# Kernel tuning notes

Hardware: AMD Instinct MI355X
Metric: run time of the kernel (lower is better)

## Reference

```python
import jax, jax.numpy as jnp
import numpy as np

H = 8          # head_num
NEG = -1e9     # mask fill value
LN_EPS = 1e-6


def setup_inputs() -> dict:
    key = jax.random.key(0)
    ks = jax.random.split(key, 12)
    B, S, D = 8, 1024, 512
    inp = {
        'q': jax.random.normal(ks[0], (B, S, D), jnp.float32),
        'k': jax.random.normal(ks[1], (B, S, D), jnp.float32),
        'v': jax.random.normal(ks[2], (B, S, D), jnp.float32),
        'query_mask': jax.random.randint(ks[3], (B, S), 0, 2, jnp.int32),
        'key_mask': jax.random.randint(ks[4], (B, S), 0, 2, jnp.int32),
        'Wq': jax.random.normal(ks[5], (D, D), jnp.float32) / np.sqrt(D),
        'bq': jax.random.normal(ks[6], (D,), jnp.float32) * 0.02,
        'Wk': jax.random.normal(ks[7], (D, D), jnp.float32) / np.sqrt(D),
        'bk': jax.random.normal(ks[8], (D,), jnp.float32) * 0.02,
        'Wv': jax.random.normal(ks[9], (D, D), jnp.float32) / np.sqrt(D),
        'bv': jax.random.normal(ks[10], (D,), jnp.float32) * 0.02,
        'gamma': jnp.ones((D,), jnp.float32),
        'beta': jnp.zeros((D,), jnp.float32),
    }
    return inp


def _to_batches(x):
    # [B,S,D] -> [B*H, S, D/H]  (batch-major head layout, as in torch code)
    B, S, D = x.shape
    return x.reshape(B, S, H, D // H).transpose(0, 2, 1, 3).reshape(B * H, S, D // H)


def _from_batches(x):
    BH, S, d = x.shape
    B = BH // H
    return x.reshape(B, H, S, d).transpose(0, 2, 1, 3).reshape(B, S, H * d)


def reference(q, k, v, query_mask, key_mask, Wq, bq, Wk, bk, Wv, bv, gamma, beta):
    # QKV linears + ReLU activation (activation=F.relu in original)
    _q = jax.nn.relu(q @ Wq.T + bq)
    _k = jax.nn.relu(k @ Wk.T + bk)
    _v = jax.nn.relu(v @ Wv.T + bv)
    _q, _k, _v = _to_batches(_q), _to_batches(_k), _to_batches(_v)  # [B*H,S,d]

    # masks tiled head-MAJOR (repeat(head_num,1) semantics): index = h*B + b
    km = jnp.tile(key_mask, (H, 1))[:, None, :]    # [B*H, 1, S_k]
    qm = jnp.tile(query_mask, (H, 1))[:, :, None]  # [B*H, S_q, 1]

    d = _q.shape[-1]
    scores = jnp.einsum('bqd,bkd->bqk', _q, _k) / jnp.sqrt(jnp.float32(d))
    scores = jnp.where(km == 0, NEG, scores)
    attn = jax.nn.softmax(scores, axis=-1)
    attn = attn * qm.astype(attn.dtype)            # multiplicative query mask
    # dropout: eval mode (rate applied only in training) -> identity
    y = jnp.einsum('bqk,bkd->bqd', attn, _v)
    y = _from_batches(y) + q                       # residual
    # LayerNorm over last dim
    mu = jnp.mean(y, axis=-1, keepdims=True)
    var = jnp.mean((y - mu) ** 2, axis=-1, keepdims=True)
    return gamma * (y - mu) / jnp.sqrt(var + LN_EPS) + beta
```

## Files before the change

kernel.cpp:

```cpp
#include <hip/hip_runtime.h>
#include <hip/hip_bf16.h>
#include <stdint.h>

constexpr int kB = 8, kH = 8, kS = 1024, kD = 512, kDH = 64;
constexpr float kNeg = -1e9f;
constexpr float kScaleLog2e = 0.125f * 1.4426950408889634f;

typedef __attribute__((ext_vector_type(8))) short bf16x8;
typedef __attribute__((ext_vector_type(8))) unsigned short u16x8;
typedef __attribute__((ext_vector_type(4))) float f32x4;
typedef __attribute__((ext_vector_type(4))) unsigned short u16x4;

__device__ __forceinline__ unsigned short f2bf(float f) {
  union { float f; unsigned int u; } a; a.f = f;
  return (unsigned short)((a.u + 0x7FFFu + ((a.u >> 16) & 1u)) >> 16);
}
__device__ __forceinline__ float bf2f(unsigned short u) {
  union { unsigned int u; float f; } a; a.u = ((unsigned int)u) << 16;
  return a.f;
}
__device__ __forceinline__ unsigned int pk2bf(float lo, float hi) {
  union { __hip_bfloat162 h; unsigned int u; } cv;
  cv.h = __float22bfloat162_rn(make_float2(lo, hi));
  return cv.u;
}
__device__ __forceinline__ uint4 gload16(const void* p) {
  uint4 r;
  asm volatile("global_load_dwordx4 %0, %1, off" : "=v"(r) : "v"(p));
  return r;
}
__device__ __forceinline__ int gload4(const void* p) {
  int r;
  asm volatile("global_load_dword %0, %1, off" : "=v"(r) : "v"(p));
  return r;
}
#define WAIT_VMCNT(N) do { \
  asm volatile("s_waitcnt vmcnt(" #N ")" ::: "memory"); \
  __builtin_amdgcn_sched_barrier(0); } while (0)

__device__ __forceinline__ uint4 cvt4(uint4 a, uint4 b) {
  uint4 r;
  r.x = pk2bf(__uint_as_float(a.x), __uint_as_float(a.y));
  r.y = pk2bf(__uint_as_float(a.z), __uint_as_float(a.w));
  r.z = pk2bf(__uint_as_float(b.x), __uint_as_float(b.y));
  r.w = pk2bf(__uint_as_float(b.z), __uint_as_float(b.w));
  return r;
}

#if __has_builtin(__builtin_amdgcn_exp2f)
#define EXP2F(x) __builtin_amdgcn_exp2f(x)
#else
#define EXP2F(x) exp2f(x)
#endif

__global__ __launch_bounds__(256)
void wcvt_kernel(const float* __restrict__ wq, const float* __restrict__ wk,
                 const float* __restrict__ wv, unsigned short* __restrict__ wout)
{
  const int tid = blockIdx.x * 256 + threadIdx.x;
  const int z = tid >> 16;
  const int i = (tid & 65535) * 4;
  const float* W = (z == 0) ? wq : (z == 1) ? wk : wv;
  float4 v4 = *(const float4*)(W + i);
  u16x4 pk;
  pk[0] = f2bf(v4.x); pk[1] = f2bf(v4.y); pk[2] = f2bf(v4.z); pk[3] = f2bf(v4.w);
  *(u16x4*)(wout + (size_t)z * 262144 + i) = pk;
}

__global__ __launch_bounds__(256)
void qkv_gemm_kernel(const float* __restrict__ xq, const float* __restrict__ xk,
                     const float* __restrict__ xv,
                     const unsigned short* __restrict__ wbf,
                     const float* __restrict__ bq, const float* __restrict__ bk,
                     const float* __restrict__ bv,
                     unsigned short* __restrict__ wsout)
{
  __shared__ __align__(16) unsigned short As[2][128][72];
  __shared__ __align__(16) unsigned short Bs[2][128][72];

  const int bid = blockIdx.x;
  const int xcd = bid & 7;
  const int j = bid >> 3;
  const int x = j & 3;
  const int g = (j >> 2) * 8 + xcd;
  const int z = g >> 6;
  const int y = g & 63;

  const float* X    = (z == 0) ? xq : (z == 1) ? xk : xv;
  const unsigned short* Wb = wbf + (size_t)z * 262144;
  const float* bias = (z == 0) ? bq : (z == 1) ? bk : bv;
  unsigned short* out = wsout + (size_t)z * (kB * kS * kD);

  const int m0 = y * 128;
  const int n0 = x * 128;
  const int t = threadIdx.x;
  const int lane = t & 63;
  const int w = t >> 6;
  const int wr = w >> 1, wc = w & 1;
  const int l16 = lane & 15, lg = lane >> 4;

  const int row = t >> 3, c8 = (t & 7) * 8;
  const float* Xr = X + (size_t)(m0 + row) * kD + c8;
  const unsigned short* Wr = Wb + (size_t)(n0 + row) * kD + c8;

  f32x4 acc[4][4] = {};
  uint4 pa0, pa1, pa2, pa3, pa4, pa5, pa6, pa7, pb0, pb1, pb2, pb3;
  uint4 qa0, qa1, qa2, qa3, qa4, qa5, qa6, qa7, qb0, qb1, qb2, qb3;

  auto issueP = [&](int kt) {
    pa0 = gload16(Xr + kt);            pa1 = gload16(Xr + kt + 4);
    pa2 = gload16(Xr + 32 * kD + kt);  pa3 = gload16(Xr + 32 * kD + kt + 4);
    pa4 = gload16(Xr + 64 * kD + kt);  pa5 = gload16(Xr + 64 * kD + kt + 4);
    pa6 = gload16(Xr + 96 * kD + kt);  pa7 = gload16(Xr + 96 * kD + kt + 4);
    pb0 = gload16(Wr + kt);            pb1 = gload16(Wr + 32 * kD + kt);
    pb2 = gload16(Wr + 64 * kD + kt);  pb3 = gload16(Wr + 96 * kD + kt);
  };
  auto issueQ = [&](int kt) {
    qa0 = gload16(Xr + kt);            qa1 = gload16(Xr + kt + 4);
    qa2 = gload16(Xr + 32 * kD + kt);  qa3 = gload16(Xr + 32 * kD + kt + 4);
    qa4 = gload16(Xr + 64 * kD + kt);  qa5 = gload16(Xr + 64 * kD + kt + 4);
    qa6 = gload16(Xr + 96 * kD + kt);  qa7 = gload16(Xr + 96 * kD + kt + 4);
    qb0 = gload16(Wr + kt);            qb1 = gload16(Wr + 32 * kD + kt);
    qb2 = gload16(Wr + 64 * kD + kt);  qb3 = gload16(Wr + 96 * kD + kt);
  };
  auto writeP = [&]() {
    *(uint4*)&As[0][row][c8]      = cvt4(pa0, pa1);
    *(uint4*)&As[0][row + 32][c8] = cvt4(pa2, pa3);
    *(uint4*)&As[0][row + 64][c8] = cvt4(pa4, pa5);
    *(uint4*)&As[0][row + 96][c8] = cvt4(pa6, pa7);
    *(uint4*)&Bs[0][row][c8]      = pb0;
    *(uint4*)&Bs[0][row + 32][c8] = pb1;
    *(uint4*)&Bs[0][row + 64][c8] = pb2;
    *(uint4*)&Bs[0][row + 96][c8] = pb3;
  };
  auto writeQ = [&]() {
    *(uint4*)&As[1][row][c8]      = cvt4(qa0, qa1);
    *(uint4*)&As[1][row + 32][c8] = cvt4(qa2, qa3);
    *(uint4*)&As[1][row + 64][c8] = cvt4(qa4, qa5);
    *(uint4*)&As[1][row + 96][c8] = cvt4(qa6, qa7);
    *(uint4*)&Bs[1][row][c8]      = qb0;
    *(uint4*)&Bs[1][row + 32][c8] = qb1;
    *(uint4*)&Bs[1][row + 64][c8] = qb2;
    *(uint4*)&Bs[1][row + 96][c8] = qb3;
  };
  auto mfma_phase = [&](int buf) {
#pragma unroll
    for (int kk = 0; kk < 2; ++kk) {
      bf16x8 av[4], bv[4];
#pragma unroll
      for (int mf = 0; mf < 4; ++mf)
        av[mf] = *(const bf16x8*)&As[buf][wr * 64 + mf * 16 + l16][kk * 32 + lg * 8];
#pragma unroll
      for (int nf = 0; nf < 4; ++nf)
        bv[nf] = *(const bf16x8*)&Bs[buf][wc * 64 + nf * 16 + l16][kk * 32 + lg * 8];
#pragma unroll
      for (int nf = 0; nf < 4; ++nf)
#pragma unroll
        for (int mf = 0; mf < 4; ++mf)
          acc[mf][nf] = __builtin_amdgcn_mfma_f32_16x16x32_bf16(bv[nf], av[mf], acc[mf][nf], 0, 0, 0);
    }
  };

  issueP(0);
  issueQ(64);
#pragma unroll
  for (int i = 0; i < 6; i += 2) {
    WAIT_VMCNT(12);
    writeP();
    issueP((i + 2) * 64);
    __syncthreads();
    mfma_phase(0);
    WAIT_VMCNT(12);
    writeQ();
    issueQ((i + 3) * 64);
    __syncthreads();
    mfma_phase(1);
  }
  WAIT_VMCNT(12);
  writeP();
  __syncthreads();
  mfma_phase(0);
  WAIT_VMCNT(0);
  writeQ();
  __syncthreads();
  mfma_phase(1);

  if (z == 2) {
    const int mmbase = m0 + wr * 64;
    const int b_ = mmbase >> 10, sbase = mmbase & 1023;
#pragma unroll
    for (int nf = 0; nf < 4; ++nf) {
#pragma unroll
      for (int r = 0; r < 4; ++r) {
        const int n = n0 + wc * 64 + nf * 16 + lg * 4 + r;
        const float bval = bias[n];
        const int h = n >> 6, dd = n & 63;
        u16x4 pk;
#pragma unroll
        for (int mf = 0; mf < 4; ++mf) {
          float vv = acc[mf][nf][r] + bval;
          vv = vv > 0.f ? vv : 0.f;
          pk[mf] = f2bf(vv);
        }
        *(u16x4*)&out[((size_t)((b_ * kH + h) * kDH + dd)) * kS + sbase + l16 * 4] = pk;
      }
    }
  } else {
#pragma unroll
    for (int mf = 0; mf < 4; ++mf) {
      const int mm = m0 + wr * 64 + mf * 16 + l16;
      const int b_ = mm >> 10, s = mm & 1023;
#pragma unroll
      for (int nf = 0; nf < 4; ++nf) {
        const int nbase = n0 + wc * 64 + nf * 16 + lg * 4;
        const int h = nbase >> 6, dd = nbase & 63;
        u16x4 pk;
#pragma unroll
        for (int r = 0; r < 4; ++r) {
          float vv = acc[mf][nf][r] + bias[nbase + r];
          vv = vv > 0.f ? vv : 0.f;
          pk[r] = f2bf(vv);
        }
        *(u16x4*)&out[((size_t)(b_ * kH + h) * kS + s) * kDH + dd] = pk;
      }
    }
  }
}

__global__ __launch_bounds__(256)
void attn_kernel(const unsigned short* __restrict__ ws,
                 const int* __restrict__ key_mask,
                 unsigned short* __restrict__ ybf)
{
  __shared__ __align__(16) unsigned short Ks[2][64][72];
  __shared__ __align__(16) unsigned short Vts[2][64][72];
  __shared__ __align__(16) unsigned short Ps[4][32][72];
  __shared__ float kmadd[2][64];

  const unsigned short* Qw = ws;
  const unsigned short* Kw = ws + (size_t)1 * kB * kS * kD;
  const unsigned short* Vw = ws + (size_t)2 * kB * kS * kD;

  const int bid = blockIdx.x;
  const int xcd = bid & 7;
  const int j = bid >> 3;
  const int qx = j & 7;
  const int bh = (j >> 3) * 8 + xcd;

  const int q0 = qx * 128;
  const int t = threadIdx.x;
  const int w = t >> 6, lane = t & 63;
  const int l16 = lane & 15, lg = lane >> 4;
  const int b_ = bh / kH, h = bh % kH;

  const unsigned short* Qb = Qw + ((size_t)bh * kS + q0) * kDH;
  const unsigned short* Kb = Kw + (size_t)bh * kS * kDH;
  const unsigned short* Vb = Vw + (size_t)bh * kDH * kS;
  const int* km = key_mask + (bh % kB) * kS;

  const int srow = t >> 3, sc8 = (t & 7) * 8;
  const unsigned short* KbR0 = Kb + (size_t)srow * kDH + sc8;
  const unsigned short* KbR1 = Kb + (size_t)(srow + 32) * kDH + sc8;
  const unsigned short* VbR0 = Vb + (size_t)srow * kS + sc8;
  const unsigned short* VbR1 = Vb + (size_t)(srow + 32) * kS + sc8;

  bf16x8 aq[2][2];
#pragma unroll
  for (int u = 0; u < 2; ++u)
#pragma unroll
    for (int kk = 0; kk < 2; ++kk)
      aq[u][kk] = *(const bf16x8*)(Qb + (size_t)(w * 32 + u * 16 + l16) * kDH + kk * 32 + lg * 8);

  bf16x8 vone;
#pragma unroll
  for (int jj = 0; jj < 8; ++jj) vone[jj] = (short)0x3F80;

  f32x4 o[2][4] = {};
  f32x4 lacc[2] = {};

  uint4 ka0, ka1, va0, va1; int kma;
  uint4 kb0, kb1, vb0, vb1; int kmb;

  auto issueA = [&](int kv0) {
    ka0 = gload16(KbR0 + (size_t)kv0 * kDH);
    ka1 = gload16(KbR1 + (size_t)kv0 * kDH);
    va0 = gload16(VbR0 + kv0);
    va1 = gload16(VbR1 + kv0);
    kma = gload4(km + kv0 + (t & 63));
  };
  auto issueB = [&](int kv0) {
    kb0 = gload16(KbR0 + (size_t)kv0 * kDH);
    kb1 = gload16(KbR1 + (size_t)kv0 * kDH);
    vb0 = gload16(VbR0 + kv0);
    vb1 = gload16(VbR1 + kv0);
    kmb = gload4(km + kv0 + (t & 63));
  };
  auto writeA = [&]() {
    *(uint4*)&Ks[0][srow][sc8]       = ka0;
    *(uint4*)&Ks[0][srow + 32][sc8]  = ka1;
    *(uint4*)&Vts[0][srow][sc8]      = va0;
    *(uint4*)&Vts[0][srow + 32][sc8] = va1;
    if (t < 64) kmadd[0][t] = kma ? 0.f : kNeg;
  };
  auto writeB = [&]() {
    *(uint4*)&Ks[1][srow][sc8]       = kb0;
    *(uint4*)&Ks[1][srow + 32][sc8]  = kb1;
    *(uint4*)&Vts[1][srow][sc8]      = vb0;
    *(uint4*)&Vts[1][srow + 32][sc8] = vb1;
    if (t < 64) kmadd[1][t] = kmb ? 0.f : kNeg;
  };
  auto compute = [&](int buf) {
    f32x4 sc[2][4] = {};
    __builtin_amdgcn_s_setprio(1);
#pragma unroll
    for (int kk = 0; kk < 2; ++kk) {
#pragma unroll
      for (int nf = 0; nf < 4; ++nf) {
        bf16x8 bfr = *(const bf16x8*)&Ks[buf][nf * 16 + l16][kk * 32 + lg * 8];
#pragma unroll
        for (int u = 0; u < 2; ++u)
          sc[u][nf] = __builtin_amdgcn_mfma_f32_16x16x32_bf16(aq[u][kk], bfr, sc[u][nf], 0, 0, 0);
      }
    }
    __builtin_amdgcn_s_setprio(0);
    float madd[4];
#pragma unroll
    for (int nf = 0; nf < 4; ++nf) madd[nf] = kmadd[buf][nf * 16 + l16];
#pragma unroll
    for (int u = 0; u < 2; ++u) {
#pragma unroll
      for (int r = 0; r < 4; ++r) {
        const float p0 = EXP2F(fmaf(sc[u][0][r], kScaleLog2e, madd[0]));
        const float p1 = EXP2F(fmaf(sc[u][1][r], kScaleLog2e, madd[1]));
        const float p2 = EXP2F(fmaf(sc[u][2][r], kScaleLog2e, madd[2]));
        const float p3 = EXP2F(fmaf(sc[u][3][r], kScaleLog2e, madd[3]));
        const int prow = u * 16 + lg * 4 + r;
        uint2 pw;
        pw.x = __builtin_amdgcn_perm(__float_as_uint(p1), __float_as_uint(p0), 0x07060302u);
        pw.y = __builtin_amdgcn_perm(__float_as_uint(p3), __float_as_uint(p2), 0x07060302u);
        *(uint2*)&Ps[w][prow][l16 * 4] = pw;
      }
    }
    __builtin_amdgcn_s_setprio(1);
#pragma unroll
    for (int kk = 0; kk < 2; ++kk) {
      bf16x8 a0 = *(const bf16x8*)&Ps[w][l16][kk * 32 + lg * 8];
      bf16x8 a1 = *(const bf16x8*)&Ps[w][16 + l16][kk * 32 + lg * 8];
#pragma unroll
      for (int nd = 0; nd < 4; ++nd) {
        bf16x8 bfr = *(const bf16x8*)&Vts[buf][nd * 16 + l16][kk * 32 + lg * 8];
        o[0][nd] = __builtin_amdgcn_mfma_f32_16x16x32_bf16(a0, bfr, o[0][nd], 0, 0, 0);
        o[1][nd] = __builtin_amdgcn_mfma_f32_16x16x32_bf16(a1, bfr, o[1][nd], 0, 0, 0);
      }
      lacc[0] = __builtin_amdgcn_mfma_f32_16x16x32_bf16(a0, vone, lacc[0], 0, 0, 0);
      lacc[1] = __builtin_amdgcn_mfma_f32_16x16x32_bf16(a1, vone, lacc[1], 0, 0, 0);
    }
    __builtin_amdgcn_s_setprio(0);
  };

  issueA(0);
  issueB(64);
  for (int i = 0; i < 14; i += 2) {
    WAIT_VMCNT(5);
    writeA();
    issueA((i + 2) * 64);
    __syncthreads();
    compute(0);
    WAIT_VMCNT(5);
    writeB();
    issueB((i + 3) * 64);
    __syncthreads();
    compute(1);
  }
  WAIT_VMCNT(5);
  writeA();
  __syncthreads();
  compute(0);
  WAIT_VMCNT(0);
  writeB();
  __syncthreads();
  compute(1);

#pragma unroll
  for (int u = 0; u < 2; ++u) {
    float rinv[4];
#pragma unroll
    for (int r = 0; r < 4; ++r) rinv[r] = 1.f / lacc[u][r];
#pragma unroll
    for (int nd = 0; nd < 4; ++nd) {
#pragma unroll
      for (int r = 0; r < 4; ++r) {
        const int srowq = q0 + w * 32 + u * 16 + lg * 4 + r;
        ybf[((size_t)b_ * kS + srowq) * kD + h * kDH + nd * 16 + l16] =
            f2bf(o[u][nd][r] * rinv[r]);
      }
    }
  }
}

__global__ __launch_bounds__(256)
void ln_kernel(const unsigned short* __restrict__ ybf, const float* __restrict__ q,
               const int* __restrict__ qmask,
               const float* __restrict__ gamma, const float* __restrict__ beta,
               float* __restrict__ out)
{
  const int w = threadIdx.x >> 6, lane = threadIdx.x & 63;
  const int row = blockIdx.x * 4 + w;
  const int b_ = row >> 10, s = row & 1023;
  const int d0 = lane * 8;
  const int h = d0 >> 6;

  const unsigned short* yp = ybf + (size_t)row * kD + d0;
  const float* qp = q + (size_t)row * kD + d0;
  const int qm = qmask[((b_ * kH + h) % kB) * kS + s];

  u16x8 yv = *(const u16x8*)yp;
  float4 q0 = *(const float4*)qp, q1 = *(const float4*)(qp + 4);
  float vals[8];
#pragma unroll
  for (int jj = 0; jj < 8; ++jj) vals[jj] = bf2f(yv[jj]);
  float qs[8]   = { q0.x, q0.y, q0.z, q0.w, q1.x, q1.y, q1.z, q1.w };

  float sum = 0.f, ss = 0.f;
#pragma unroll
  for (int jj = 0; jj < 8; ++jj) {
    const float val = (qm ? vals[jj] : 0.f) + qs[jj];
    vals[jj] = val; sum += val; ss += val * val;
  }
#pragma unroll
  for (int off = 1; off < 64; off <<= 1) {
    sum += __shfl_xor(sum, off);
    ss  += __shfl_xor(ss, off);
  }
  const float mu = sum * (1.f / kD);
  const float var = ss * (1.f / kD) - mu * mu;
  const float rstd = rsqrtf(var + 1e-6f);

  float4 g0 = *(const float4*)(gamma + d0), g1 = *(const float4*)(gamma + d0 + 4);
  float4 be0 = *(const float4*)(beta + d0), be1 = *(const float4*)(beta + d0 + 4);
  float gs[8] = { g0.x, g0.y, g0.z, g0.w, g1.x, g1.y, g1.z, g1.w };
  float bs[8] = { be0.x, be0.y, be0.z, be0.w, be1.x, be1.y, be1.z, be1.w };

  float4 o0, o1;
  o0.x = gs[0] * (vals[0] - mu) * rstd + bs[0];
  o0.y = gs[1] * (vals[1] - mu) * rstd + bs[1];
  o0.z = gs[2] * (vals[2] - mu) * rstd + bs[2];
  o0.w = gs[3] * (vals[3] - mu) * rstd + bs[3];
  o1.x = gs[4] * (vals[4] - mu) * rstd + bs[4];
  o1.y = gs[5] * (vals[5] - mu) * rstd + bs[5];
  o1.z = gs[6] * (vals[6] - mu) * rstd + bs[6];
  o1.w = gs[7] * (vals[7] - mu) * rstd + bs[7];
  *(float4*)(out + (size_t)row * kD + d0) = o0;
  *(float4*)(out + (size_t)row * kD + d0 + 4) = o1;
}

extern "C" void kernel_launch(void* const* d_in, const int* in_sizes, int n_in,
                              void* d_out, int out_size, void* d_ws, size_t ws_size,
                              hipStream_t stream) {
  const float* q  = (const float*)d_in[0];
  const float* k  = (const float*)d_in[1];
  const float* v  = (const float*)d_in[2];
  const int* qmask = (const int*)d_in[3];
  const int* kmask = (const int*)d_in[4];
  const float* Wq = (const float*)d_in[5];
  const float* bq = (const float*)d_in[6];
  const float* Wk = (const float*)d_in[7];
  const float* bk = (const float*)d_in[8];
  const float* Wv = (const float*)d_in[9];
  const float* bv = (const float*)d_in[10];
  const float* gamma = (const float*)d_in[11];
  const float* beta  = (const float*)d_in[12];
  float* out = (float*)d_out;
  unsigned short* wsqkv = (unsigned short*)d_ws;
  unsigned short* ybf   = wsqkv + (size_t)3 * 4194304;
  unsigned short* wbf   = (unsigned short*)d_out;

  wcvt_kernel<<<768, 256, 0, stream>>>(Wq, Wk, Wv, wbf);
  qkv_gemm_kernel<<<768, 256, 0, stream>>>(
      q, k, v, wbf, bq, bk, bv, wsqkv);
  attn_kernel<<<512, 256, 0, stream>>>(wsqkv, kmask, ybf);
  ln_kernel<<<2048, 256, 0, stream>>>(ybf, q, qmask, gamma, beta, out);
}
```

Baseline: 70.50 us.

## Interleave global prefetch with MFMA sub-phases and raise wave priority in QKV GEMM

Splits each k-tile MFMA phase of the QKV projection GEMM into four sub-phases. Each sub-phase issues a quarter of the next tile's global loads, then runs its MFMAs under s_setprio(1), with barriers between sub-phases. The aim is to spread memory issue across compute and keep waves in lockstep for better MFMA utilisation. The cost is three extra __syncthreads per phase and more register pressure from the partially issued load groups.

```diff
diff --git a/kernel.cpp b/kernel.cpp
--- a/kernel.cpp
+++ b/kernel.cpp
@@ -123,6 +123,38 @@
     qb0 = gload16(Wr + kt);            qb1 = gload16(Wr + 32 * kD + kt);
     qb2 = gload16(Wr + 64 * kD + kt);  qb3 = gload16(Wr + 96 * kD + kt);
   };
+  auto issueP1 = [&](int kt) {
+    pa0 = gload16(Xr + kt);            pa1 = gload16(Xr + kt + 4);
+    pa2 = gload16(Xr + 32 * kD + kt);
+  };
+  auto issueP2 = [&](int kt) {
+    pa3 = gload16(Xr + 32 * kD + kt + 4);
+    pa4 = gload16(Xr + 64 * kD + kt);  pa5 = gload16(Xr + 64 * kD + kt + 4);
+  };
+  auto issueP3 = [&](int kt) {
+    pa6 = gload16(Xr + 96 * kD + kt);  pa7 = gload16(Xr + 96 * kD + kt + 4);
+    pb0 = gload16(Wr + kt);
+  };
+  auto issueP4 = [&](int kt) {
+    pb1 = gload16(Wr + 32 * kD + kt);
+    pb2 = gload16(Wr + 64 * kD + kt);  pb3 = gload16(Wr + 96 * kD + kt);
+  };
+  auto issueQ1 = [&](int kt) {
+    qa0 = gload16(Xr + kt);            qa1 = gload16(Xr + kt + 4);
+    qa2 = gload16(Xr + 32 * kD + kt);
+  };
+  auto issueQ2 = [&](int kt) {
+    qa3 = gload16(Xr + 32 * kD + kt + 4);
+    qa4 = gload16(Xr + 64 * kD + kt);  qa5 = gload16(Xr + 64 * kD + kt + 4);
+  };
+  auto issueQ3 = [&](int kt) {
+    qa6 = gload16(Xr + 96 * kD + kt);  qa7 = gload16(Xr + 96 * kD + kt + 4);
+    qb0 = gload16(Wr + kt);
+  };
+  auto issueQ4 = [&](int kt) {
+    qb1 = gload16(Wr + 32 * kD + kt);
+    qb2 = gload16(Wr + 64 * kD + kt);  qb3 = gload16(Wr + 96 * kD + kt);
+  };
   auto writeP = [&]() {
     *(uint4*)&As[0][row][c8]      = cvt4(pa0, pa1);
     *(uint4*)&As[0][row + 32][c8] = cvt4(pa2, pa3);
@@ -143,23 +175,78 @@
     *(uint4*)&Bs[1][row + 64][c8] = qb2;
     *(uint4*)&Bs[1][row + 96][c8] = qb3;
   };
-  auto mfma_phase = [&](int buf) {
-#pragma unroll
-    for (int kk = 0; kk < 2; ++kk) {
-      bf16x8 av[4], bv[4];
-#pragma unroll
-      for (int mf = 0; mf < 4; ++mf)
-        av[mf] = *(const bf16x8*)&As[buf][wr * 64 + mf * 16 + l16][kk * 32 + lg * 8];
-#pragma unroll
-      for (int nf = 0; nf < 4; ++nf)
-        bv[nf] = *(const bf16x8*)&Bs[buf][wc * 64 + nf * 16 + l16][kk * 32 + lg * 8];
-#pragma unroll
-      for (int nf = 0; nf < 4; ++nf)
-#pragma unroll
-        for (int mf = 0; mf < 4; ++mf)
-          acc[mf][nf] = __builtin_amdgcn_mfma_f32_16x16x32_bf16(bv[nf], av[mf], acc[mf][nf], 0, 0, 0);
-    }
-  };
+
+#define COMPUTE_PHASED(BUF, KT, I1, I2, I3, I4)                               \
+  do {                                                                        \
+    bf16x8 av0, av1, av2, av3, bv0, bv1;                                      \
+                                                   \
+    av0 = *(const bf16x8*)&As[BUF][wr * 64 +  0 + l16][lg * 8];               \
+    av1 = *(const bf16x8*)&As[BUF][wr * 64 + 16 + l16][lg * 8];               \
+    av2 = *(const bf16x8*)&As[BUF][wr * 64 + 32 + l16][lg * 8];               \
+    av3 = *(const bf16x8*)&As[BUF][wr * 64 + 48 + l16][lg * 8];               \
+    bv0 = *(const bf16x8*)&Bs[BUF][wc * 64 +  0 + l16][lg * 8];               \
+    bv1 = *(const bf16x8*)&Bs[BUF][wc * 64 + 16 + l16][lg * 8];               \
+    if (KT >= 0) I1(KT);                                                      \
+    __builtin_amdgcn_s_setprio(1);                                            \
+    acc[0][0] = __builtin_amdgcn_mfma_f32_16x16x32_bf16(bv0, av0, acc[0][0], 0, 0, 0); \
+    acc[1][0] = __builtin_amdgcn_mfma_f32_16x16x32_bf16(bv0, av1, acc[1][0], 0, 0, 0); \
+    acc[2][0] = __builtin_amdgcn_mfma_f32_16x16x32_bf16(bv0, av2, acc[2][0], 0, 0, 0); \
+    acc[3][0] = __builtin_amdgcn_mfma_f32_16x16x32_bf16(bv0, av3, acc[3][0], 0, 0, 0); \
+    acc[0][1] = __builtin_amdgcn_mfma_f32_16x16x32_bf16(bv1, av0, acc[0][1], 0, 0, 0); \
+    acc[1][1] = __builtin_amdgcn_mfma_f32_16x16x32_bf16(bv1, av1, acc[1][1], 0, 0, 0); \
+    acc[2][1] = __builtin_amdgcn_mfma_f32_16x16x32_bf16(bv1, av2, acc[2][1], 0, 0, 0); \
+    acc[3][1] = __builtin_amdgcn_mfma_f32_16x16x32_bf16(bv1, av3, acc[3][1], 0, 0, 0); \
+    __builtin_amdgcn_s_setprio(0);                                            \
+    __syncthreads();                                                          \
+                                                   \
+    bv0 = *(const bf16x8*)&Bs[BUF][wc * 64 + 32 + l16][lg * 8];               \
+    bv1 = *(const bf16x8*)&Bs[BUF][wc * 64 + 48 + l16][lg * 8];               \
+    if (KT >= 0) I2(KT);                                                      \
+    __builtin_amdgcn_s_setprio(1);                                            \
+    acc[0][2] = __builtin_amdgcn_mfma_f32_16x16x32_bf16(bv0, av0, acc[0][2], 0, 0, 0); \
+    acc[1][2] = __builtin_amdgcn_mfma_f32_16x16x32_bf16(bv0, av1, acc[1][2], 0, 0, 0); \
+    acc[2][2] = __builtin_amdgcn_mfma_f32_16x16x32_bf16(bv0, av2, acc[2][2], 0, 0, 0); \
+    acc[3][2] = __builtin_amdgcn_mfma_f32_16x16x32_bf16(bv0, av3, acc[3][2], 0, 0, 0); \
+    acc[0][3] = __builtin_amdgcn_mfma_f32_16x16x32_bf16(bv1, av0, acc[0][3], 0, 0, 0); \
+    acc[1][3] = __builtin_amdgcn_mfma_f32_16x16x32_bf16(bv1, av1, acc[1][3], 0, 0, 0); \
+    acc[2][3] = __builtin_amdgcn_mfma_f32_16x16x32_bf16(bv1, av2, acc[2][3], 0, 0, 0); \
+    acc[3][3] = __builtin_amdgcn_mfma_f32_16x16x32_bf16(bv1, av3, acc[3][3], 0, 0, 0); \
+    __builtin_amdgcn_s_setprio(0);                                            \
+    __syncthreads();                                                          \
+                                                   \
+    av0 = *(const bf16x8*)&As[BUF][wr * 64 +  0 + l16][32 + lg * 8];          \
+    av1 = *(const bf16x8*)&As[BUF][wr * 64 + 16 + l16][32 + lg * 8];          \
+    av2 = *(const bf16x8*)&As[BUF][wr * 64 + 32 + l16][32 + lg * 8];          \
+    av3 = *(const bf16x8*)&As[BUF][wr * 64 + 48 + l16][32 + lg * 8];          \
+    bv0 = *(const bf16x8*)&Bs[BUF][wc * 64 +  0 + l16][32 + lg * 8];          \
+    bv1 = *(const bf16x8*)&Bs[BUF][wc * 64 + 16 + l16][32 + lg * 8];          \
+    if (KT >= 0) I3(KT);                                                      \
+    __builtin_amdgcn_s_setprio(1);                                            \
+    acc[0][0] = __builtin_amdgcn_mfma_f32_16x16x32_bf16(bv0, av0, acc[0][0], 0, 0, 0); \
+    acc[1][0] = __builtin_amdgcn_mfma_f32_16x16x32_bf16(bv0, av1, acc[1][0], 0, 0, 0); \
+    acc[2][0] = __builtin_amdgcn_mfma_f32_16x16x32_bf16(bv0, av2, acc[2][0], 0, 0, 0); \
+    acc[3][0] = __builtin_amdgcn_mfma_f32_16x16x32_bf16(bv0, av3, acc[3][0], 0, 0, 0); \
+    acc[0][1] = __builtin_amdgcn_mfma_f32_16x16x32_bf16(bv1, av0, acc[0][1], 0, 0, 0); \
+    acc[1][1] = __builtin_amdgcn_mfma_f32_16x16x32_bf16(bv1, av1, acc[1][1], 0, 0, 0); \
+    acc[2][1] = __builtin_amdgcn_mfma_f32_16x16x32_bf16(bv1, av2, acc[2][1], 0, 0, 0); \
+    acc[3][1] = __builtin_amdgcn_mfma_f32_16x16x32_bf16(bv1, av3, acc[3][1], 0, 0, 0); \
+    __builtin_amdgcn_s_setprio(0);                                            \
+    __syncthreads();                                                          \
+                                                   \
+    bv0 = *(const bf16x8*)&Bs[BUF][wc * 64 + 32 + l16][32 + lg * 8];          \
+    bv1 = *(const bf16x8*)&Bs[BUF][wc * 64 + 48 + l16][32 + lg * 8];          \
+    if (KT >= 0) I4(KT);                                                      \
+    __builtin_amdgcn_s_setprio(1);                                            \
+    acc[0][2] = __builtin_amdgcn_mfma_f32_16x16x32_bf16(bv0, av0, acc[0][2], 0, 0, 0); \
+    acc[1][2] = __builtin_amdgcn_mfma_f32_16x16x32_bf16(bv0, av1, acc[1][2], 0, 0, 0); \
+    acc[2][2] = __builtin_amdgcn_mfma_f32_16x16x32_bf16(bv0, av2, acc[2][2], 0, 0, 0); \
+    acc[3][2] = __builtin_amdgcn_mfma_f32_16x16x32_bf16(bv0, av3, acc[3][2], 0, 0, 0); \
+    acc[0][3] = __builtin_amdgcn_mfma_f32_16x16x32_bf16(bv1, av0, acc[0][3], 0, 0, 0); \
+    acc[1][3] = __builtin_amdgcn_mfma_f32_16x16x32_bf16(bv1, av1, acc[1][3], 0, 0, 0); \
+    acc[2][3] = __builtin_amdgcn_mfma_f32_16x16x32_bf16(bv1, av2, acc[2][3], 0, 0, 0); \
+    acc[3][3] = __builtin_amdgcn_mfma_f32_16x16x32_bf16(bv1, av3, acc[3][3], 0, 0, 0); \
+    __builtin_amdgcn_s_setprio(0);                                            \
+  } while (0)
 
   issueP(0);
   issueQ(64);
@@ -167,23 +254,22 @@
   for (int i = 0; i < 6; i += 2) {
     WAIT_VMCNT(12);
     writeP();
-    issueP((i + 2) * 64);
     __syncthreads();
-    mfma_phase(0);
+    COMPUTE_PHASED(0, (i + 2) * 64, issueP1, issueP2, issueP3, issueP4);
     WAIT_VMCNT(12);
     writeQ();
-    issueQ((i + 3) * 64);
     __syncthreads();
-    mfma_phase(1);
+    COMPUTE_PHASED(1, (i + 3) * 64, issueQ1, issueQ2, issueQ3, issueQ4);
   }
   WAIT_VMCNT(12);
   writeP();
   __syncthreads();
-  mfma_phase(0);
+  COMPUTE_PHASED(0, -1, issueP1, issueP2, issueP3, issueP4);
   WAIT_VMCNT(0);
   writeQ();
   __syncthreads();
-  mfma_phase(1);
+  COMPUTE_PHASED(1, -1, issueQ1, issueQ2, issueQ3, issueQ4);
+#undef COMPUTE_PHASED
 
   if (z == 2) {
     const int mmbase = m0 + wr * 64;
```

Result: faster. 68.96 us (-2.2%).

## Restructure QKV GEMM into phased single-buffer pipeline and retune attention LDS padding

Applied to the files above, without the earlier changes.

Replaces the QKV GEMM's two LDS buffers and two register prefetch sets with one LDS buffer. The next tile's global loads are split into four chunks, each issued between MFMA groups, with s_setprio raised around the MFMAs and barriers between phases. The aim is to overlap memory traffic with matrix math while cutting LDS and register use, at the cost of a shallower prefetch and extra barriers. Attention LDS row padding changes from 72 to 68 elements, which leaves 16-byte vector reads misaligned on odd rows. The bf16 weight scratch also moves from the output buffer into the workspace.

```diff
diff --git a/kernel.cpp b/kernel.cpp
--- a/kernel.cpp
+++ b/kernel.cpp
@@ -75,8 +75,8 @@
                      const float* __restrict__ bv,
                      unsigned short* __restrict__ wsout)
 {
-  __shared__ __align__(16) unsigned short As[2][128][72];
-  __shared__ __align__(16) unsigned short Bs[2][128][72];
+  __shared__ __align__(16) unsigned short As[128][72];
+  __shared__ __align__(16) unsigned short Bs[128][72];
 
   const int bid = blockIdx.x;
   const int xcd = bid & 7;
@@ -105,9 +105,8 @@
 
   f32x4 acc[4][4] = {};
   uint4 pa0, pa1, pa2, pa3, pa4, pa5, pa6, pa7, pb0, pb1, pb2, pb3;
-  uint4 qa0, qa1, qa2, qa3, qa4, qa5, qa6, qa7, qb0, qb1, qb2, qb3;
-
-  auto issueP = [&](int kt) {
+
+  auto issueAll = [&](int kt) {
     pa0 = gload16(Xr + kt);            pa1 = gload16(Xr + kt + 4);
     pa2 = gload16(Xr + 32 * kD + kt);  pa3 = gload16(Xr + 32 * kD + kt + 4);
     pa4 = gload16(Xr + 64 * kD + kt);  pa5 = gload16(Xr + 64 * kD + kt + 4);
@@ -115,75 +114,109 @@
     pb0 = gload16(Wr + kt);            pb1 = gload16(Wr + 32 * kD + kt);
     pb2 = gload16(Wr + 64 * kD + kt);  pb3 = gload16(Wr + 96 * kD + kt);
   };
-  auto issueQ = [&](int kt) {
-    qa0 = gload16(Xr + kt);            qa1 = gload16(Xr + kt + 4);
-    qa2 = gload16(Xr + 32 * kD + kt);  qa3 = gload16(Xr + 32 * kD + kt + 4);
-    qa4 = gload16(Xr + 64 * kD + kt);  qa5 = gload16(Xr + 64 * kD + kt + 4);
-    qa6 = gload16(Xr + 96 * kD + kt);  qa7 = gload16(Xr + 96 * kD + kt + 4);
-    qb0 = gload16(Wr + kt);            qb1 = gload16(Wr + 32 * kD + kt);
-    qb2 = gload16(Wr + 64 * kD + kt);  qb3 = gload16(Wr + 96 * kD + kt);
-  };
-  auto writeP = [&]() {
-    *(uint4*)&As[0][row][c8]      = cvt4(pa0, pa1);
-    *(uint4*)&As[0][row + 32][c8] = cvt4(pa2, pa3);
-    *(uint4*)&As[0][row + 64][c8] = cvt4(pa4, pa5);
-    *(uint4*)&As[0][row + 96][c8] = cvt4(pa6, pa7);
-    *(uint4*)&Bs[0][row][c8]      = pb0;
-    *(uint4*)&Bs[0][row + 32][c8] = pb1;
-    *(uint4*)&Bs[0][row + 64][c8] = pb2;
-    *(uint4*)&Bs[0][row + 96][c8] = pb3;
-  };
-  auto writeQ = [&]() {
-    *(uint4*)&As[1][row][c8]      = cvt4(qa0, qa1);
-    *(uint4*)&As[1][row + 32][c8] = cvt4(qa2, qa3);
-    *(uint4*)&As[1][row + 64][c8] = cvt4(qa4, qa5);
-    *(uint4*)&As[1][row + 96][c8] = cvt4(qa6, qa7);
-    *(uint4*)&Bs[1][row][c8]      = qb0;
-    *(uint4*)&Bs[1][row + 32][c8] = qb1;
-    *(uint4*)&Bs[1][row + 64][c8] = qb2;
-    *(uint4*)&Bs[1][row + 96][c8] = qb3;
-  };
-  auto mfma_phase = [&](int buf) {
-#pragma unroll
-    for (int kk = 0; kk < 2; ++kk) {
-      bf16x8 av[4], bv[4];
-#pragma unroll
-      for (int mf = 0; mf < 4; ++mf)
-        av[mf] = *(const bf16x8*)&As[buf][wr * 64 + mf * 16 + l16][kk * 32 + lg * 8];
-#pragma unroll
-      for (int nf = 0; nf < 4; ++nf)
-        bv[nf] = *(const bf16x8*)&Bs[buf][wc * 64 + nf * 16 + l16][kk * 32 + lg * 8];
-#pragma unroll
-      for (int nf = 0; nf < 4; ++nf)
-#pragma unroll
-        for (int mf = 0; mf < 4; ++mf)
-          acc[mf][nf] = __builtin_amdgcn_mfma_f32_16x16x32_bf16(bv[nf], av[mf], acc[mf][nf], 0, 0, 0);
-    }
-  };
-
-  issueP(0);
-  issueQ(64);
-#pragma unroll
-  for (int i = 0; i < 6; i += 2) {
-    WAIT_VMCNT(12);
-    writeP();
-    issueP((i + 2) * 64);
-    __syncthreads();
-    mfma_phase(0);
-    WAIT_VMCNT(12);
-    writeQ();
-    issueQ((i + 3) * 64);
-    __syncthreads();
-    mfma_phase(1);
+  auto issue1 = [&](int kt) {
+    pa0 = gload16(Xr + kt);            pa1 = gload16(Xr + kt + 4);
+    pa2 = gload16(Xr + 32 * kD + kt);
+  };
+  auto issue2 = [&](int kt) {
+    pa3 = gload16(Xr + 32 * kD + kt + 4);
+    pa4 = gload16(Xr + 64 * kD + kt);  pa5 = gload16(Xr + 64 * kD + kt + 4);
+  };
+  auto issue3 = [&](int kt) {
+    pa6 = gload16(Xr + 96 * kD + kt);  pa7 = gload16(Xr + 96 * kD + kt + 4);
+    pb0 = gload16(Wr + kt);
+  };
+  auto issue4 = [&](int kt) {
+    pb1 = gload16(Wr + 32 * kD + kt);
+    pb2 = gload16(Wr + 64 * kD + kt);  pb3 = gload16(Wr + 96 * kD + kt);
+  };
+  auto lds_write = [&]() {
+    *(uint4*)&As[row][c8]      = cvt4(pa0, pa1);
+    *(uint4*)&As[row + 32][c8] = cvt4(pa2, pa3);
+    *(uint4*)&As[row + 64][c8] = cvt4(pa4, pa5);
+    *(uint4*)&As[row + 96][c8] = cvt4(pa6, pa7);
+    *(uint4*)&Bs[row][c8]      = pb0;
+    *(uint4*)&Bs[row + 32][c8] = pb1;
+    *(uint4*)&Bs[row + 64][c8] = pb2;
+    *(uint4*)&Bs[row + 96][c8] = pb3;
+  };
+
+  auto compute_phased = [&](int KT) {
+    bf16x8 av0, av1, av2, av3, bv0, bv1;
+    av0 = *(const bf16x8*)&As[wr * 64 +  0 + l16][lg * 8];
+    av1 = *(const bf16x8*)&As[wr * 64 + 16 + l16][lg * 8];
+    av2 = *(const bf16x8*)&As[wr * 64 + 32 + l16][lg * 8];
+    av3 = *(const bf16x8*)&As[wr * 64 + 48 + l16][lg * 8];
+    bv0 = *(const bf16x8*)&Bs[wc * 64 +  0 + l16][lg * 8];
+    bv1 = *(const bf16x8*)&Bs[wc * 64 + 16 + l16][lg * 8];
+    if (KT >= 0) issue1(KT);
+    __builtin_amdgcn_s_setprio(1);
+    acc[0][0] = __builtin_amdgcn_mfma_f32_16x16x32_bf16(bv0, av0, acc[0][0], 0, 0, 0);
+    acc[1][0] = __builtin_amdgcn_mfma_f32_16x16x32_bf16(bv0, av1, acc[1][0], 0, 0, 0);
+    acc[2][0] = __builtin_amdgcn_mfma_f32_16x16x32_bf16(bv0, av2, acc[2][0], 0, 0, 0);
+    acc[3][0] = __builtin_amdgcn_mfma_f32_16x16x32_bf16(bv0, av3, acc[3][0], 0, 0, 0);
+    acc[0][1] = __builtin_amdgcn_mfma_f32_16x16x32_bf16(bv1, av0, acc[0][1], 0, 0, 0);
+    acc[1][1] = __builtin_amdgcn_mfma_f32_16x16x32_bf16(bv1, av1, acc[1][1], 0, 0, 0);
+    acc[2][1] = __builtin_amdgcn_mfma_f32_16x16x32_bf16(bv1, av2, acc[2][1], 0, 0, 0);
+    acc[3][1] = __builtin_amdgcn_mfma_f32_16x16x32_bf16(bv1, av3, acc[3][1], 0, 0, 0);
+    __builtin_amdgcn_s_setprio(0);
+    __syncthreads();
+    bv0 = *(const bf16x8*)&Bs[wc * 64 + 32 + l16][lg * 8];
+    bv1 = *(const bf16x8*)&Bs[wc * 64 + 48 + l16][lg * 8];
+    if (KT >= 0) issue2(KT);
+    __builtin_amdgcn_s_setprio(1);
+    acc[0][2] = __builtin_amdgcn_mfma_f32_16x16x32_bf16(bv0, av0, acc[0][2], 0, 0, 0);
+    acc[1][2] = __builtin_amdgcn_mfma_f32_16x16x32_bf16(bv0, av1, acc[1][2], 0, 0, 0);
+    acc[2][2] = __builtin_amdgcn_mfma_f32_16x16x32_bf16(bv0, av2, acc[2][2], 0, 0, 0);
+    acc[3][2] = __builtin_amdgcn_mfma_f32_16x16x32_bf16(bv0, av3, acc[3][2], 0, 0, 0);
+    acc[0][3] = __builtin_amdgcn_mfma_f32_16x16x32_bf16(bv1, av0, acc[0][3], 0, 0, 0);
+    acc[1][3] = __builtin_amdgcn_mfma_f32_16x16x32_bf16(bv1, av1, acc[1][3], 0, 0, 0);
+    acc[2][3] = __builtin_amdgcn_mfma_f32_16x16x32_bf16(bv1, av2, acc[2][3], 0, 0, 0);
+    acc[3][3] = __builtin_amdgcn_mfma_f32_16x16x32_bf16(bv1, av3, acc[3][3], 0, 0, 0);
+    __builtin_amdgcn_s_setprio(0);
+    __syncthreads();
+    av0 = *(const bf16x8*)&As[wr * 64 +  0 + l16][32 + lg * 8];
+    av1 = *(const bf16x8*)&As[wr * 64 + 16 + l16][32 + lg * 8];
+    av2 = *(const bf16x8*)&As[wr * 64 + 32 + l16][32 + lg * 8];
+    av3 = *(const bf16x8*)&As[wr * 64 + 48 + l16][32 + lg * 8];
+    bv0 = *(const bf16x8*)&Bs[wc * 64 +  0 + l16][32 + lg * 8];
+    bv1 = *(const bf16x8*)&Bs[wc * 64 + 16 + l16][32 + lg * 8];
+    if (KT >= 0) issue3(KT);
+    __builtin_amdgcn_s_setprio(1);
+    acc[0][0] = __builtin_amdgcn_mfma_f32_16x16x32_bf16(bv0, av0, acc[0][0], 0, 0, 0);
+    acc[1][0] = __builtin_amdgcn_mfma_f32_16x16x32_bf16(bv0, av1, acc[1][0], 0, 0, 0);
+    acc[2][0] = __builtin_amdgcn_mfma_f32_16x16x32_bf16(bv0, av2, acc[2][0], 0, 0, 0);
+    acc[3][0] = __builtin_amdgcn_mfma_f32_16x16x32_bf16(bv0, av3, acc[3][0], 0, 0, 0);
+    acc[0][1] = __builtin_amdgcn_mfma_f32_16x16x32_bf16(bv1, av0, acc[0][1], 0, 0, 0);
+    acc[1][1] = __builtin_amdgcn_mfma_f32_16x16x32_bf16(bv1, av1, acc[1][1], 0, 0, 0);
+    acc[2][1] = __builtin_amdgcn_mfma_f32_16x16x32_bf16(bv1, av2, acc[2][1], 0, 0, 0);
+    acc[3][1] = __builtin_amdgcn_mfma_f32_16x16x32_bf16(bv1, av3, acc[3][1], 0, 0, 0);
+    __builtin_amdgcn_s_setprio(0);
+    __syncthreads();
+    bv0 = *(const bf16x8*)&Bs[wc * 64 + 32 + l16][32 + lg * 8];
+    bv1 = *(const bf16x8*)&Bs[wc * 64 + 48 + l16][32 + lg * 8];
+    if (KT >= 0) issue4(KT);
+    __builtin_amdgcn_s_setprio(1);
+    acc[0][2] = __builtin_amdgcn_mfma_f32_16x16x32_bf16(bv0, av0, acc[0][2], 0, 0, 0);
+    acc[1][2] = __builtin_amdgcn_mfma_f32_16x16x32_bf16(bv0, av1, acc[1][2], 0, 0, 0);
+    acc[2][2] = __builtin_amdgcn_mfma_f32_16x16x32_bf16(bv0, av2, acc[2][2], 0, 0, 0);
+    acc[3][2] = __builtin_amdgcn_mfma_f32_16x16x32_bf16(bv0, av3, acc[3][2], 0, 0, 0);
+    acc[0][3] = __builtin_amdgcn_mfma_f32_16x16x32_bf16(bv1, av0, acc[0][3], 0, 0, 0);
+    acc[1][3] = __builtin_amdgcn_mfma_f32_16x16x32_bf16(bv1, av1, acc[1][3], 0, 0, 0);
+    acc[2][3] = __builtin_amdgcn_mfma_f32_16x16x32_bf16(bv1, av2, acc[2][3], 0, 0, 0);
+    acc[3][3] = __builtin_amdgcn_mfma_f32_16x16x32_bf16(bv1, av3, acc[3][3], 0, 0, 0);
+    __builtin_amdgcn_s_setprio(0);
+  };
+
+  issueAll(0);
+#pragma unroll
+  for (int i = 0; i < 8; ++i) {
+    WAIT_VMCNT(0);
+    lds_write();
+    __syncthreads();
+    compute_phased(i < 7 ? (i + 1) * 64 : -1);
+    __syncthreads();
   }
-  WAIT_VMCNT(12);
-  writeP();
-  __syncthreads();
-  mfma_phase(0);
-  WAIT_VMCNT(0);
-  writeQ();
-  __syncthreads();
-  mfma_phase(1);
 
   if (z == 2) {
     const int mmbase = m0 + wr * 64;
@@ -232,9 +265,9 @@
                  const int* __restrict__ key_mask,
                  unsigned short* __restrict__ ybf)
 {
-  __shared__ __align__(16) unsigned short Ks[2][64][72];
-  __shared__ __align__(16) unsigned short Vts[2][64][72];
-  __shared__ __align__(16) unsigned short Ps[4][32][72];
+  __shared__ __align__(16) unsigned short Ks[2][64][68];
+  __shared__ __align__(16) unsigned short Vts[2][64][68];
+  __shared__ __align__(16) unsigned short Ps[4][32][68];
   __shared__ float kmadd[2][64];
 
   const unsigned short* Qw = ws;
@@ -473,7 +506,7 @@
   float* out = (float*)d_out;
   unsigned short* wsqkv = (unsigned short*)d_ws;
   unsigned short* ybf   = wsqkv + (size_t)3 * 4194304;
-  unsigned short* wbf   = (unsigned short*)d_out;
+  unsigned short* wbf   = wsqkv + (size_t)4 * 4194304;
 
   wcvt_kernel<<<768, 256, 0, stream>>>(Wq, Wk, Wv, wbf);
   qkv_gemm_kernel<<<768, 256, 0, stream>>>(
```

New measurement: 71.66 us. Within noise of the previous version (+1.6%).
